# Kernel optimization log

Hardware: AMD Instinct MI355X
Metric: run time of the kernel (lower is better)

## Reference

```python
import jax, jax.numpy as jnp
import numpy as np

B, P, D_ENC, D_DEC, D_ATT, E, V, T = 64, 144, 1792, 512, 512, 300, 32000, 30
LN_EPS = 1e-5


def _ln(x, g, b):
    m = x.mean(-1, keepdims=True)
    v = jnp.var(x, axis=-1, keepdims=True)
    return (x - m) * jax.lax.rsqrt(v + LN_EPS) * g + b


def setup_inputs() -> dict:
    key = jax.random.key(0)
    ks = iter(jax.random.split(key, 40))
    r = lambda shape, s=0.02: (jax.random.normal(next(ks), shape, jnp.float32) * s)
    inp = {}
    inp['features'] = jax.random.normal(next(ks), (B, P, D_ENC), jnp.float32)
    inp['captions'] = jax.random.randint(next(ks), (B, T), 0, V, jnp.int32)
    inp['emb_table'] = r((V, E), 0.05)
    # attention params
    inp['ln_q_g'] = jnp.ones((D_DEC,), jnp.float32)
    inp['ln_q_b'] = jnp.zeros((D_DEC,), jnp.float32)
    inp['ln_kv_g'] = jnp.ones((D_ENC,), jnp.float32)
    inp['ln_kv_b'] = jnp.zeros((D_ENC,), jnp.float32)
    inp['Wq'] = r((D_DEC, D_ATT)); inp['bq'] = jnp.zeros((D_ATT,), jnp.float32)
    inp['Wk'] = r((D_ENC, D_ATT)); inp['bk'] = jnp.zeros((D_ATT,), jnp.float32)
    inp['Wbeta'] = r((D_DEC, 1)); inp['bbeta'] = jnp.zeros((1,), jnp.float32)
    # LSTM gate params, packed as [in_dim, 4*H] in gate order (i, f, o, g).
    # Context fed to the LSTM is the attention output of dim encoder_dim (V = normalized features).
    inp['Wh'] = r((D_DEC, 4 * D_DEC))
    inp['Wu'] = r((E, 4 * D_DEC))
    inp['Wa'] = r((D_ENC, 4 * D_DEC))
    inp['b_gates'] = jnp.zeros((4 * D_DEC,), jnp.float32)  # linear biases + extra b_* params combined
    # output head
    inp['W_Lh'] = r((D_DEC, E)); inp['b_Lh'] = jnp.zeros((E,), jnp.float32)
    inp['W_Lz'] = r((D_ENC, E)); inp['b_Lz'] = jnp.zeros((E,), jnp.float32)
    inp['W_Lo'] = r((E, V)); inp['b_Lo'] = jnp.zeros((V,), jnp.float32)
    # init state
    inp['W_ih'] = r((D_ENC, D_DEC)); inp['b_ih'] = jnp.zeros((D_DEC,), jnp.float32)
    inp['W_ic'] = r((D_ENC, D_DEC)); inp['b_ic'] = jnp.zeros((D_DEC,), jnp.float32)
    return inp


def reference(features, captions, emb_table, ln_q_g, ln_q_b, ln_kv_g, ln_kv_b,
              Wq, bq, Wk, bk, Wbeta, bbeta, Wh, Wu, Wa, b_gates,
              W_Lh, b_Lh, W_Lz, b_Lz, W_Lo, b_Lo, W_ih, b_ih, W_ic, b_ic):
    scale = jnp.sqrt(jnp.asarray(Wq.shape[1], jnp.float32))
    # features are constant across timesteps -> hoist ln_kv and K projection
    feats_n = _ln(features, ln_kv_g, ln_kv_b)          # [B,P,Denc]
    K = feats_n @ Wk + bk                               # [B,P,A]
    mean_a = features.mean(axis=1)                      # [B,Denc]
    h0 = mean_a @ W_ih + b_ih
    c0 = mean_a @ W_ic + b_ic
    embs = emb_table[captions]                          # [B,T,E] (dropout = identity in eval)
    xs = jnp.swapaxes(embs[:, :-1], 0, 1)               # [T-1,B,E], embedding at step t is word t-1

    def step(carry, emb_t):
        h, c = carry
        hq = _ln(h, ln_q_g, ln_q_b)                     # [B,H]
        Q = hq @ Wq + bq                                # [B,A]
        scores = jnp.einsum('ba,bpa->bp', Q, K) / scale
        alpha = jax.nn.softmax(scores, axis=-1)         # [B,P]
        context = jnp.einsum('bp,bpd->bd', alpha, feats_n)  # [B,Denc]
        beta = jax.nn.sigmoid(hq @ Wbeta + bbeta)       # [B,1]
        z = beta * context
        gates = h @ Wh + emb_t @ Wu + z @ Wa + b_gates  # [B,4H]
        i_t, f_t, o_t, g_t = jnp.split(gates, 4, axis=-1)
        c_new = jax.nn.sigmoid(f_t) * c + jax.nn.sigmoid(i_t) * jnp.tanh(g_t)
        h_new = jax.nn.sigmoid(o_t) * jnp.tanh(c_new)
        out_o = emb_t + (h_new @ W_Lh + b_Lh) + (z @ W_Lz + b_Lz)
        logits = out_o @ W_Lo + b_Lo                    # [B,V]
        return (h_new, c_new), (logits, alpha)

    _, (logits, alphas) = jax.lax.scan(step, (h0, c0), xs)
    # step t=0 stays zero, as in the original torch loop (range(1, seq_len))
    predictions = jnp.concatenate(
        [jnp.zeros((1,) + logits.shape[1:], logits.dtype), logits], axis=0).swapaxes(0, 1)
    alphas_out = jnp.concatenate(
        [jnp.zeros((1,) + alphas.shape[1:], alphas.dtype), alphas], axis=0).swapaxes(0, 1)
    return predictions, alphas_out
```

## Files before the change

kernel.cpp:

```cpp
#include <hip/hip_runtime.h>
#include <hip/hip_bf16.h>


#define NB 64
#define NP 144
#define DE 1792
#define DD 512
#define DA 512
#define EM 300
#define NV 32000
#define NTT 30
#define NS 29
#define G4 2048
#define KP 320
#define KG1 2304
#define LN_EPS 1e-5f
#define RSCALE 0.044194173824159216f
#define KSPL 12

typedef __attribute__((ext_vector_type(8))) short short8;
typedef __attribute__((ext_vector_type(4))) float f32x4;
typedef __attribute__((ext_vector_type(8))) unsigned short ushort8v;

__device__ __forceinline__ float bf2f(unsigned short u){
  union { unsigned int i; float f; } w; w.i = ((unsigned int)u) << 16; return w.f;
}
__device__ __forceinline__ unsigned short f2bf(float f){
  union { float f; unsigned int i; } u; u.f = f;
  unsigned int r = u.i + 0x7FFFu + ((u.i >> 16) & 1u);
  return (unsigned short)(r >> 16);
}
__device__ __forceinline__ float sigm(float x){ return 1.f/(1.f + __expf(-x)); }

__device__ __forceinline__ float wave_reduce_sum(float v){
  #pragma unroll
  for (int o = 32; o >= 1; o >>= 1) v += __shfl_xor(v, o);
  return v;
}
__device__ __forceinline__ float wave_reduce_max(float v){
  #pragma unroll
  for (int o = 32; o >= 1; o >>= 1) v = fmaxf(v, __shfl_xor(v, o));
  return v;
}
__device__ __forceinline__ float block_sum256(float v, float* sbuf){
  v = wave_reduce_sum(v);
  const int lane = threadIdx.x & 63, wid = threadIdx.x >> 6;
  if (lane == 0) sbuf[wid] = v;
  __syncthreads();
  const float r = sbuf[0] + sbuf[1] + sbuf[2] + sbuf[3];
  __syncthreads();
  return r;
}
__device__ __forceinline__ float block_sum512(float v, float* sbuf8){
  v = wave_reduce_sum(v);
  const int lane = threadIdx.x & 63, wid = threadIdx.x >> 6;
  if (lane == 0) sbuf8[wid] = v;
  __syncthreads();
  float r = 0.f;
  #pragma unroll
  for (int i = 0; i < 8; ++i) r += sbuf8[i];
  __syncthreads();
  return r;
}

__device__ __forceinline__ void stage_tile(const unsigned short* __restrict__ src,
    int row_stride, int k0, char* lds){
  const int tid = threadIdx.x;
  #pragma unroll
  for (int c = 0; c < 2; ++c){
    const int o = tid + c*256;
    const int m = o >> 3, ks8 = o & 7;
    const ushort8v v = *(const ushort8v*)&src[(size_t)m*row_stride + k0 + ks8*8];
    *(ushort8v*)&lds[m*128 + ((ks8 ^ (m&7))<<4)] = v;
  }
}
__device__ __forceinline__ void mma64(const char* Alds, const char* Blds,
    int w, int lane, f32x4 acc[4]){
  #pragma unroll
  for (int ks = 0; ks < 2; ++ks){
    const int slot = ks*4 + (lane>>4);
    const int n = w*16 + (lane&15);
    const short8 bfv = *(const short8*)&Blds[n*128 + ((slot ^ (n&7))<<4)];
    #pragma unroll
    for (int fm = 0; fm < 4; ++fm){
      const int m = fm*16 + (lane&15);
      const short8 afv = *(const short8*)&Alds[m*128 + ((slot ^ (m&7))<<4)];
      acc[fm] = __builtin_amdgcn_mfma_f32_16x16x32_bf16(afv, bfv, acc[fm], 0, 0, 0);
    }
  }
}

template <int NKT>
__device__ __forceinline__ void gemm_big(const unsigned short* __restrict__ A,
    const unsigned short* __restrict__ B, int sa, int sb,
    char* Alds, char* Blds, int mt, int nt, f32x4 acc[8][4]){
  const int tid = threadIdx.x, w = tid>>6, lane = tid&63;
  for (int kt = 0; kt < NKT; ++kt){
    const int k0 = kt*64;
    __syncthreads();
    #pragma unroll
    for (int c2 = 0; c2 < 4; ++c2){
      const int o16 = tid + c2*256;
      const int m = o16>>3, ks8 = o16&7;
      const ushort8v v = *(const ushort8v*)&A[(size_t)(mt*128+m)*sa + k0 + ks8*8];
      *(ushort8v*)&Alds[m*128 + ((ks8 ^ (m&7))<<4)] = v;
    }
    #pragma unroll
    for (int c2 = 0; c2 < 8; ++c2){
      const int o16 = tid + c2*256;
      const int n = o16>>3, ks8 = o16&7;
      const ushort8v v = *(const ushort8v*)&B[(size_t)(nt*256+n)*sb + k0 + ks8*8];
      *(ushort8v*)&Blds[n*128 + ((ks8 ^ (n&7))<<4)] = v;
    }
    __syncthreads();
    #pragma unroll
    for (int ks = 0; ks < 2; ++ks){
      const int slot = ks*4 + (lane>>4);
      short8 af[8];
      #pragma unroll
      for (int fm = 0; fm < 8; ++fm){
        const int m = fm*16 + (lane&15);
        af[fm] = *(const short8*)&Alds[m*128 + ((slot ^ (m&7))<<4)];
      }
      #pragma unroll
      for (int fn = 0; fn < 4; ++fn){
        const int n = w*64 + fn*16 + (lane&15);
        const short8 bfv = *(const short8*)&Blds[n*128 + ((slot ^ (n&7))<<4)];
        #pragma unroll
        for (int fm = 0; fm < 8; ++fm)
          acc[fm][fn] = __builtin_amdgcn_mfma_f32_16x16x32_bf16(af[fm], bfv, acc[fm][fn], 0, 0, 0);
      }
    }
  }
}

__global__ __launch_bounds__(256) void k_zero(float* __restrict__ pred,
                                              float* __restrict__ alph){
  const int idx = blockIdx.x * 256 + threadIdx.x;
  {
    const int b = idx / NV, v = idx - b * NV;
    pred[(size_t)b * NTT * NV + v] = 0.f;
  }
  if (idx < NB * NP){
    const int b = idx / NP, p = idx - b * NP;
    alph[(size_t)b * NTT * NP + p] = 0.f;
  }
}

__global__ __launch_bounds__(256) void k_ln_feats(const float* __restrict__ feats,
    const float* __restrict__ g, const float* __restrict__ bb,
    unsigned short* __restrict__ out){
  __shared__ float sbuf[4];
  const int row = blockIdx.x;
  const float* x = feats + (size_t)row * DE;
  float v[7]; float s = 0.f;
  #pragma unroll
  for (int i = 0; i < 7; ++i){ v[i] = x[i*256 + threadIdx.x]; s += v[i]; }
  const float mean = block_sum256(s, sbuf) * (1.f/DE);
  float q = 0.f;
  #pragma unroll
  for (int i = 0; i < 7; ++i){ const float d = v[i] - mean; q += d*d; }
  const float var = block_sum256(q, sbuf) * (1.f/DE);
  const float rinv = rsqrtf(var + LN_EPS);
  #pragma unroll
  for (int i = 0; i < 7; ++i){
    const int idx = i*256 + threadIdx.x;
    out[(size_t)row*DE + idx] = f2bf((v[i]-mean)*rinv*g[idx] + bb[idx]);
  }
}

__global__ __launch_bounds__(256) void k_mean(const float* __restrict__ feats,
                                              float* __restrict__ mean_a){
  const int idx = blockIdx.x * 256 + threadIdx.x;
  const int b = idx / DE, d = idx - b * DE;
  const float* p = feats + (size_t)b * NP * DE + d;
  float s = 0.f;
  for (int pp = 0; pp < NP; ++pp) s += p[(size_t)pp * DE];
  mean_a[idx] = s * (1.f/NP);
}

__global__ __launch_bounds__(256) void k_cvt_T(const float* __restrict__ src,
    unsigned short* __restrict__ dst, const int K, const int N, const int KPad){
  __shared__ float t[64][65];
  const int n0 = blockIdx.x*64, k0 = blockIdx.y*64;
  for (int i = threadIdx.x; i < 4096; i += 256){
    const int k = i>>6, n = i&63;
    t[k][n] = (k0 + k < K) ? src[(size_t)(k0+k)*N + n0+n] : 0.f;
  }
  __syncthreads();
  for (int i = threadIdx.x; i < 4096; i += 256){
    const int n = i>>6, k = i&63;
    dst[(size_t)(n0+n)*KPad + k0+k] = f2bf(t[k][n]);
  }
}

__global__ __launch_bounds__(256) void k_cvt_wlt(const float* __restrict__ W_Lh,
    const float* __restrict__ W_Lz, unsigned short* __restrict__ WLt){
  __shared__ float t[64][65];
  const int e0 = blockIdx.x*64, k0 = blockIdx.y*64;
  for (int i = threadIdx.x; i < 4096; i += 256){
    const int k = i>>6, e2 = i&63;
    const int kg = k0 + k, e = e0 + e2;
    float v = 0.f;
    if (e < EM) v = (kg < DD) ? W_Lh[(size_t)kg*EM + e] : W_Lz[(size_t)(kg-DD)*EM + e];
    t[k][e2] = v;
  }
  __syncthreads();
  for (int i = threadIdx.x; i < 4096; i += 256){
    const int e2 = i>>6, k = i&63;
    WLt[(size_t)(e0+e2)*KG1 + k0+k] = f2bf(t[k][e2]);
  }
}

__global__ __launch_bounds__(256) void k_wg(const float* __restrict__ Wq,
    const float* __restrict__ g, unsigned short* __restrict__ Wg){
  const int idx = blockIdx.x*256 + threadIdx.x;
  const int k = idx >> 9;
  Wg[idx] = f2bf(g[k]*Wq[idx]);
}

__global__ __launch_bounds__(512) void k_pre_vq(const float* __restrict__ Wq,
    const float* __restrict__ bk, float* __restrict__ vq){
  const int k = threadIdx.x;
  const float* row = Wq + (size_t)k*DA;
  float acc = 0.f;
  for (int a = 0; a < DA; ++a) acc = fmaf(row[a], bk[a], acc);
  vq[k] = acc;
}

__global__ __launch_bounds__(512) void k_uvoff(const float* __restrict__ Wq,
    const float* __restrict__ g, const float* __restrict__ bln,
    const float* __restrict__ bq, const float* __restrict__ Wbeta,
    const float* __restrict__ bbeta, const float* __restrict__ bk,
    float* __restrict__ u_, float* __restrict__ voff,
    float* __restrict__ gw, float* __restrict__ cscal){
  __shared__ float sbuf8[8];
  const int a = threadIdx.x;
  float uu = 0.f, vv = 0.f;
  for (int k = 0; k < DD; ++k){
    const float wv = Wq[(size_t)k*DA + a];
    uu = fmaf(g[k],   wv, uu);
    vv = fmaf(bln[k], wv, vv);
  }
  const float vo = vv + bq[a];
  u_[a]   = uu;
  voff[a] = vo;
  gw[a]   = g[a]*Wbeta[a];
  const float c1 = block_sum512(g[a]*Wbeta[a], sbuf8);
  const float c2 = block_sum512(bln[a]*Wbeta[a], sbuf8);
  const float c3 = block_sum512(uu*bk[a], sbuf8);
  const float c4 = block_sum512(vo*bk[a], sbuf8);
  if (a == 0){ cscal[0]=c1; cscal[1]=c2+bbeta[0]; cscal[2]=c3; cscal[3]=c4; }
}

__global__ __launch_bounds__(256) void k_KF(const unsigned short* __restrict__ fb,
    const unsigned short* __restrict__ WkT, unsigned short* __restrict__ KF){
  __shared__ char Alds[128*128];
  __shared__ char Blds[256*128];
  const int bid = blockIdx.x;
  const int wgid = (bid & 7)*18 + (bid >> 3);
  const int nt = wgid & 1, mt = wgid >> 1;
  const int tid = threadIdx.x, w = tid>>6, lane = tid&63;
  f32x4 acc[8][4];
  #pragma unroll
  for (int i = 0; i < 8; ++i)
    #pragma unroll
    for (int j = 0; j < 4; ++j) acc[i][j] = (f32x4)(0.f);
  gemm_big<28>(fb, WkT, DE, DE, Alds, Blds, mt, nt, acc);
  const int ncol0 = nt*256 + w*64 + (lane&15);
  #pragma unroll
  for (int fm = 0; fm < 8; ++fm)
    #pragma unroll
    for (int r = 0; r < 4; ++r){
      const int row = mt*128 + fm*16 + (lane>>4)*4 + r;
      #pragma unroll
      for (int fn = 0; fn < 4; ++fn)
        KF[(size_t)row*DD + ncol0 + fn*16] = f2bf(acc[fm][fn][r]);
    }
}

__global__ __launch_bounds__(256) void k_QG2(const unsigned short* __restrict__ KF,
    const unsigned short* __restrict__ Wg, const float* __restrict__ g_,
    const float* __restrict__ vq, unsigned short* __restrict__ G2){
  __shared__ char Alds[128*128];
  __shared__ char Blds[256*128];
  const int bid = blockIdx.x;
  const int wgid = (bid & 7)*18 + (bid >> 3);
  const int nt = wgid & 1, mt = wgid >> 1;
  const int tid = threadIdx.x, w = tid>>6, lane = tid&63;
  f32x4 acc[8][4];
  #pragma unroll
  for (int i = 0; i < 8; ++i)
    #pragma unroll
    for (int j = 0; j < 4; ++j) acc[i][j] = (f32x4)(0.f);
  gemm_big<8>(KF, Wg, DD, DD, Alds, Blds, mt, nt, acc);
  const int ncol0 = nt*256 + w*64 + (lane&15);
  float addv[4];
  #pragma unroll
  for (int fn = 0; fn < 4; ++fn){
    const int q = ncol0 + fn*16;
    addv[fn] = g_[q]*vq[q];
  }
  #pragma unroll
  for (int fm = 0; fm < 8; ++fm)
    #pragma unroll
    for (int r = 0; r < 4; ++r){
      const int row = mt*128 + fm*16 + (lane>>4)*4 + r;
      #pragma unroll
      for (int fn = 0; fn < 4; ++fn)
        G2[(size_t)row*DD + ncol0 + fn*16] = f2bf(acc[fm][fn][r] + addv[fn]);
    }
}

__global__ __launch_bounds__(512) void k_sc12(const unsigned short* __restrict__ KF,
    const float* __restrict__ u_, const float* __restrict__ voff,
    const float* __restrict__ cscal, float2* __restrict__ sc12){
  const int w = threadIdx.x>>6, lane = threadIdx.x&63;
  const int row = blockIdx.x*8 + w;
  const unsigned short* kf = KF + (size_t)row*DD + lane*8;
  float s1 = 0.f, s2 = 0.f;
  #pragma unroll
  for (int j = 0; j < 8; ++j){
    const float kv = bf2f(kf[j]);
    s1 = fmaf(u_[lane*8 + j],   kv, s1);
    s2 = fmaf(voff[lane*8 + j], kv, s2);
  }
  s1 = wave_reduce_sum(s1);
  s2 = wave_reduce_sum(s2);
  if (lane == 0){
    float2 o; o.x = s1 + cscal[2]; o.y = s2 + cscal[3];
    sc12[row] = o;
  }
}

__global__ __launch_bounds__(256) void k_init_g(const float* __restrict__ mean_a,
    const float* __restrict__ W, const float* __restrict__ bias,
    float* __restrict__ out, unsigned short* __restrict__ outbf){
  __shared__ float la[64*68];
  __shared__ float lb[64*68];
  const int j0 = blockIdx.x*64;
  const int tid = threadIdx.x, tr = tid&15, tn = tid>>4;
  float acc[16] = {0.f};
  for (int a0 = 0; a0 < DE; a0 += 64){
    __syncthreads();
    for (int i = tid; i < 4096; i += 256){
      const int b = i>>6, k = i&63;
      la[k*68 + b] = mean_a[(size_t)b*DE + a0+k];
    }
    for (int i = tid; i < 4096; i += 256){
      const int k = i>>6, j = i&63;
      lb[k*68 + j] = W[(size_t)(a0+k)*DD + j0+j];
    }
    __syncthreads();
    for (int k = 0; k < 64; ++k){
      float av[4], bv[4];
      #pragma unroll
      for (int ii = 0; ii < 4; ++ii) av[ii] = la[k*68 + tr*4+ii];
      #pragma unroll
      for (int jj = 0; jj < 4; ++jj) bv[jj] = lb[k*68 + tn*4+jj];
      #pragma unroll
      for (int ii = 0; ii < 4; ++ii)
        #pragma unroll
        for (int jj = 0; jj < 4; ++jj)
          acc[ii*4+jj] = fmaf(av[ii], bv[jj], acc[ii*4+jj]);
    }
  }
  #pragma unroll
  for (int ii = 0; ii < 4; ++ii)
    #pragma unroll
    for (int jj = 0; jj < 4; ++jj){
      const size_t idx = (size_t)(tr*4+ii)*DD + j0 + tn*4+jj;
      const float val = acc[ii*4+jj] + bias[j0 + tn*4+jj];
      out[idx] = val;
      if (outbf) outbf[idx] = f2bf(val);
    }
}

__global__ __launch_bounds__(256) void k_EU(const float* __restrict__ emb_table,
    const int* __restrict__ captions, const unsigned short* __restrict__ wut,
    float* __restrict__ eu){
  __shared__ char Alds[8192];
  __shared__ char Blds[8192];
  __shared__ int capL[64];
  const int jt = blockIdx.x, s = blockIdx.y;
  const int tid = threadIdx.x, w = tid>>6, lane = tid&63;
  if (tid < 64) capL[tid] = captions[tid*NTT + s];
  f32x4 acc[4];
  #pragma unroll
  for (int i = 0; i < 4; ++i) acc[i] = (f32x4)(0.f);
  for (int kt = 0; kt < 5; ++kt){
    __syncthreads();
    #pragma unroll
    for (int c = 0; c < 2; ++c){
      const int o = tid + c*256;
      const int m = o>>3, ks8 = o&7;
      const int e0 = kt*64 + ks8*8;
      const float* er = emb_table + (size_t)capL[m]*EM;
      ushort8v v;
      #pragma unroll
      for (int jj = 0; jj < 8; ++jj)
        v[jj] = (e0 + jj < EM) ? f2bf(er[e0 + jj]) : (unsigned short)0;
      *(ushort8v*)&Alds[m*128 + ((ks8 ^ (m&7))<<4)] = v;
    }
    stage_tile(wut + (size_t)jt*64*KP, KP, kt*64, Blds);
    __syncthreads();
    mma64(Alds, Blds, w, lane, acc);
  }
  const int j = jt*64 + w*16 + (lane&15);
  #pragma unroll
  for (int fm = 0; fm < 4; ++fm)
    #pragma unroll
    for (int r = 0; r < 4; ++r){
      const int b = fm*16 + (lane>>4)*4 + r;
      eu[((size_t)s*NB + b)*G4 + j] = acc[fm][r];
    }
}

__global__ __launch_bounds__(512) void k_A(
    const unsigned short* __restrict__ gp, const float* __restrict__ eu,
    const float* __restrict__ b_gates, const float* __restrict__ cin,
    float* __restrict__ cout, unsigned short* __restrict__ hst,
    const unsigned short* __restrict__ G2, const float2* __restrict__ sc12,
    const unsigned short* __restrict__ fb, const float* __restrict__ gw,
    const float* __restrict__ cscal, const int s, const int do_att,
    float* __restrict__ alph, unsigned short* __restrict__ zbf){
  __shared__ alignas(16) unsigned short hL[DD];
  __shared__ float sc[NP];
  __shared__ float al[NP];
  __shared__ float sredA[8*4];
  __shared__ float sbufM[8];
  __shared__ float sbufS[8];
  int sl, b;
  if (gridDim.x == 1){ sl = 0; b = blockIdx.y; }
  else {
    const int lin = blockIdx.x + 2*blockIdx.y;
    const int xcd = lin & 7, i = lin >> 3;
    b = xcd*8 + (i & 7);
    sl = i >> 3;
  }
  const int tid = threadIdx.x;
  const int w = tid>>6, lane = tid&63;
  float hn;
  if (s == 0){
    const unsigned short hb = hst[(size_t)b*DD + tid];
    hn = bf2f(hb);
    hL[tid] = hb;
  } else {
    const int m = s - 1;
    unsigned short gv[4*KSPL];
    #pragma unroll
    for (int ks = 0; ks < KSPL; ++ks){
      const unsigned short* gr = gp + ((size_t)ks*NB + b)*G4 + tid;
      gv[ks*4+0] = gr[0];
      gv[ks*4+1] = gr[DD];
      gv[ks*4+2] = gr[2*DD];
      gv[ks*4+3] = gr[3*DD];
    }
    const float* eur = eu + ((size_t)m*NB + b)*G4 + tid;
    float gs0 = b_gates[tid]        + eur[0];
    float gs1 = b_gates[DD + tid]   + eur[DD];
    float gs2 = b_gates[2*DD + tid] + eur[2*DD];
    float gs3 = b_gates[3*DD + tid] + eur[3*DD];
    #pragma unroll
    for (int ks = 0; ks < KSPL; ++ks){
      gs0 += bf2f(gv[ks*4+0]); gs1 += bf2f(gv[ks*4+1]);
      gs2 += bf2f(gv[ks*4+2]); gs3 += bf2f(gv[ks*4+3]);
    }
    const size_t idx = (size_t)b*DD + tid;
    const float cn = sigm(gs1)*cin[idx] + sigm(gs0)*tanhf(gs3);
    hn = sigm(gs2)*tanhf(cn);
    cout[idx] = cn;
    const unsigned short hb = f2bf(hn);
    hst[(size_t)s*NB*DD + idx] = hb;
    hL[tid] = hb;
  }
  if (!do_att) return;
  float p1 = hn, p2 = hn*hn, p3 = hn*gw[tid];
  #pragma unroll
  for (int o = 32; o >= 1; o >>= 1){
    p1 += __shfl_xor(p1, o);
    p2 += __shfl_xor(p2, o);
    p3 += __shfl_xor(p3, o);
  }
  if (lane == 0){ sredA[w*4] = p1; sredA[w*4+1] = p2; sredA[w*4+2] = p3; }
  __syncthreads();
  float S1 = 0.f, S2 = 0.f, S3 = 0.f;
  #pragma unroll
  for (int i = 0; i < 8; ++i){
    S1 += sredA[i*4]; S2 += sredA[i*4+1]; S3 += sredA[i*4+2];
  }
  const float mean = S1*(1.f/512.f);
  const float var  = S2*(1.f/512.f) - mean*mean;
  const float rinv = rsqrtf(var + LN_EPS);
  const float beta = sigm(rinv*(S3 - mean*cscal[0]) + cscal[1]);
  const short8 hv = *(const short8*)&hL[lane*8];
  #pragma unroll 1
  for (int i0 = 0; i0 < 18; i0 += 9){
    short8 U[9];
    float2 SV[9];
    #pragma unroll
    for (int j = 0; j < 9; ++j){
      const int p = w + 8*(i0+j);
      U[j] = *(const short8*)&G2[(size_t)(b*NP + p)*DD + lane*8];
      if (lane == 0) SV[j] = sc12[b*NP + p];
    }
    #pragma unroll
    for (int j = 0; j < 9; ++j){
      float a2 = 0.f;
      #pragma unroll
      for (int q = 0; q < 8; ++q)
        a2 = fmaf(bf2f((unsigned short)U[j][q]), bf2f((unsigned short)hv[q]), a2);
      a2 = wave_reduce_sum(a2);
      if (lane == 0)
        sc[w + 8*(i0+j)] = RSCALE*(rinv*a2 - rinv*mean*SV[j].x + SV[j].y);
    }
  }
  __syncthreads();
  const float v = (tid < NP) ? sc[tid] : -1e30f;
  const float mv = wave_reduce_max(v);
  if (lane == 0) sbufM[w] = mv;
  __syncthreads();
  float mm = sbufM[0];
  #pragma unroll
  for (int i = 1; i < 8; ++i) mm = fmaxf(mm, sbufM[i]);
  const float e = (tid < NP) ? __expf(v - mm) : 0.f;
  const float sv = wave_reduce_sum(e);
  if (lane == 0) sbufS[w] = sv;
  __syncthreads();
  float ssum = 0.f;
  #pragma unroll
  for (int i = 0; i < 8; ++i) ssum += sbufS[i];
  if (tid < NP){
    const float a3 = e / ssum;
    al[tid] = a3;
    if (sl == 0) alph[((size_t)b*NTT + s + 1)*NP + tid] = a3;
  }
  __syncthreads();
  if (tid < 448){
    const int d0 = sl*896 + tid*2;
    const unsigned short* fB = fb + (size_t)b*NP*DE + d0;
    float a0 = 0.f, a1 = 0.f;
    #pragma unroll 1
    for (int p0 = 0; p0 < NP; p0 += 36){
      ushort2 fv[36];
      #pragma unroll
      for (int j = 0; j < 36; ++j) fv[j] = *(const ushort2*)&fB[(size_t)(p0+j)*DE];
      #pragma unroll
      for (int j = 0; j < 36; ++j){
        const float ap = al[p0+j];
        a0 = fmaf(ap, bf2f(fv[j].x), a0);
        a1 = fmaf(ap, bf2f(fv[j].y), a1);
      }
    }
    ushort2 zo;
    zo.x = f2bf(a0*beta);
    zo.y = f2bf(a1*beta);
    *(ushort2*)&zbf[((size_t)s*NB + b)*DE + d0] = zo;
  }
}

__global__ __launch_bounds__(256) void k_B(
    const unsigned short* __restrict__ hst, const unsigned short* __restrict__ zbf,
    const unsigned short* __restrict__ whT, const unsigned short* __restrict__ wat,
    const int s, unsigned short* __restrict__ gp){
  __shared__ char Alds[8192];
  __shared__ char Blds[8192];
  const int jt = blockIdx.x, ks = blockIdx.y;
  const int tid = threadIdx.x, w = tid>>6, lane = tid&63;
  const unsigned short* hrow = hst + (size_t)s*NB*DD;
  const unsigned short* zrow = zbf + (size_t)s*NB*DE;
  f32x4 acc[4];
  #pragma unroll
  for (int i = 0; i < 4; ++i) acc[i] = (f32x4)(0.f);
  for (int kt = 0; kt < 3; ++kt){
    const int k0 = ks*192 + kt*64;
    __syncthreads();
    if (k0 < DD) stage_tile(hrow, DD, k0, Alds);
    else         stage_tile(zrow, DE, k0 - DD, Alds);
    #pragma unroll
    for (int c2 = 0; c2 < 2; ++c2){
      const int o = tid + c2*256;
      const int m = o>>3, ks8 = o&7;
      const int col = (m>>4)*DD + jt*16 + (m&15);
      const unsigned short* src = (k0 < DD)
          ? whT + (size_t)col*DD + k0
          : wat + (size_t)col*DE + (k0 - DD);
      const ushort8v v = *(const ushort8v*)&src[ks8*8];
      *(ushort8v*)&Blds[m*128 + ((ks8 ^ (m&7))<<4)] = v;
    }
    __syncthreads();
    mma64(Alds, Blds, w, lane, acc);
  }
  const int jcol = jt*16 + (lane&15);
  unsigned short* gps = gp + (size_t)ks*NB*G4;
  #pragma unroll
  for (int fm = 0; fm < 4; ++fm)
    #pragma unroll
    for (int r = 0; r < 4; ++r){
      const int b = fm*16 + (lane>>4)*4 + r;
      gps[(size_t)b*G4 + w*DD + jcol] = f2bf(acc[fm][r]);
    }
}

__global__ __launch_bounds__(256) void k_G1m(const unsigned short* __restrict__ hstbf,
    const unsigned short* __restrict__ zbf, const unsigned short* __restrict__ WLt,
    float* __restrict__ g1p){
  __shared__ char Alds[8192];
  __shared__ char Blds[8192];
  const int e0 = blockIdx.x*64, s = blockIdx.y, ks6 = blockIdx.z;
  const int tid = threadIdx.x, w = tid>>6, lane = tid&63;
  const unsigned short* hrow = hstbf + (size_t)(s+1)*NB*DD;
  const unsigned short* zrow = zbf + (size_t)s*NB*DE;
  f32x4 acc[4];
  #pragma unroll
  for (int i = 0; i < 4; ++i) acc[i] = (f32x4)(0.f);
  for (int kt = 0; kt < 6; ++kt){
    const int k0 = ks6*384 + kt*64;
    __syncthreads();
    if (k0 < DD) stage_tile(hrow, DD, k0, Alds);
    else         stage_tile(zrow, DE, k0 - DD, Alds);
    stage_tile(WLt + (size_t)e0*KG1, KG1, k0, Blds);
    __syncthreads();
    mma64(Alds, Blds, w, lane, acc);
  }
  const int e = e0 + w*16 + (lane&15);
  float* dst = g1p + (size_t)ks6*NS*NB*KP;
  #pragma unroll
  for (int fm = 0; fm < 4; ++fm)
    #pragma unroll
    for (int r = 0; r < 4; ++r){
      const int b = fm*16 + (lane>>4)*4 + r;
      dst[((size_t)s*NB + b)*KP + e] = acc[fm][r];
    }
}

__global__ __launch_bounds__(256) void k_G1red(const float* __restrict__ g1p,
    const float* __restrict__ b_Lh, const float* __restrict__ b_Lz,
    const float* __restrict__ emb_table, const int* __restrict__ captions,
    unsigned short* __restrict__ outo){
  const int idx = blockIdx.x*256 + threadIdx.x;
  const int row = idx / KP, e = idx - row*KP;
  const int s = row >> 6, b = row & 63;
  float v = 0.f;
  #pragma unroll
  for (int ks6 = 0; ks6 < 6; ++ks6) v += g1p[(size_t)ks6*NS*NB*KP + idx];
  if (e < EM){
    const int cap = captions[b*NTT + s];
    v += b_Lh[e] + b_Lz[e] + emb_table[(size_t)cap*EM + e];
  } else v = 0.f;
  outo[idx] = f2bf(v);
}

__global__ __launch_bounds__(256) void k_G2(const unsigned short* __restrict__ Abf,
    const unsigned short* __restrict__ Bt, const float* __restrict__ b_Lo,
    float* __restrict__ pred){
  __shared__ char Alds[128*128];
  __shared__ char Blds[256*128];
  const int bid = blockIdx.x;
  const int xcd = bid & 7, idx8 = bid >> 3;
  const int wgid = (xcd < 3 ? xcd*235 : 705 + (xcd-3)*234) + idx8;
  const int nt = wgid / 15, mt = wgid - nt*15;
  const int tid = threadIdx.x, w = tid>>6, lane = tid&63;
  f32x4 acc[8][4];
  #pragma unroll
  for (int i = 0; i < 8; ++i)
    #pragma unroll
    for (int j = 0; j < 4; ++j)
      acc[i][j] = (f32x4)(0.f);
  gemm_big<5>(Abf, Bt, KP, KP, Alds, Blds, mt, nt, acc);
  const int ncol0 = nt*256 + w*64 + (lane&15);
  #pragma unroll
  for (int fm = 0; fm < 8; ++fm){
    #pragma unroll
    for (int r = 0; r < 4; ++r){
      const int row = mt*128 + fm*16 + (lane>>4)*4 + r;
      if (row < NS*NB){
        const int s = row >> 6, b = row & 63;
        float* prow = &pred[((size_t)b*NTT + s + 1)*NV + ncol0];
        #pragma unroll
        for (int fn = 0; fn < 4; ++fn)
          __builtin_nontemporal_store(acc[fm][fn][r] + b_Lo[ncol0 + fn*16],
                                      &prow[fn*16]);
      }
    }
  }
}

extern "C" void kernel_launch(void* const* d_in, const int* in_sizes, int n_in,
                              void* d_out, int out_size, void* d_ws, size_t ws_size,
                              hipStream_t stream){
  const float* features  = (const float*)d_in[0];
  const int*   captions  = (const int*)  d_in[1];
  const float* emb_table = (const float*)d_in[2];
  const float* ln_q_g = (const float*)d_in[3];
  const float* ln_q_b = (const float*)d_in[4];
  const float* ln_kv_g= (const float*)d_in[5];
  const float* ln_kv_b= (const float*)d_in[6];
  const float* Wq     = (const float*)d_in[7];
  const float* bq     = (const float*)d_in[8];
  const float* Wk     = (const float*)d_in[9];
  const float* bk     = (const float*)d_in[10];
  const float* Wbeta  = (const float*)d_in[11];
  const float* bbeta  = (const float*)d_in[12];
  const float* Wh     = (const float*)d_in[13];
  const float* Wu     = (const float*)d_in[14];
  const float* Wa     = (const float*)d_in[15];
  const float* b_gates= (const float*)d_in[16];
  const float* W_Lh   = (const float*)d_in[17];
  const float* b_Lh   = (const float*)d_in[18];
  const float* W_Lz   = (const float*)d_in[19];
  const float* b_Lz   = (const float*)d_in[20];
  const float* W_Lo   = (const float*)d_in[21];
  const float* b_Lo   = (const float*)d_in[22];
  const float* W_ih   = (const float*)d_in[23];
  const float* b_ih   = (const float*)d_in[24];
  const float* W_ic   = (const float*)d_in[25];
  const float* b_ic   = (const float*)d_in[26];

  float* pred = (float*)d_out;
  float* alph = pred + (size_t)NB * NTT * NV;

  char* w = (char*)d_ws;
  auto alloc = [&](size_t bytes) -> void* {
    void* p = (void*)w; w += (bytes + 255) & ~(size_t)255; return p;
  };
  unsigned short* feats_bf = (unsigned short*)alloc((size_t)NB*NP*DE * 2);
  unsigned short* wlo_t    = (unsigned short*)alloc((size_t)NV*KP * 2);
  unsigned short* whT      = (unsigned short*)alloc((size_t)G4*DD * 2);
  unsigned short* wut      = (unsigned short*)alloc((size_t)G4*KP * 2);
  unsigned short* wat      = (unsigned short*)alloc((size_t)G4*DE * 2);
  unsigned short* WkT      = (unsigned short*)alloc((size_t)DD*DE * 2);
  unsigned short* WLt      = (unsigned short*)alloc((size_t)KP*KG1 * 2);
  unsigned short* Wg       = (unsigned short*)alloc((size_t)DD*DD * 2);
  unsigned short* KFbf     = (unsigned short*)alloc((size_t)NB*NP*DD * 2);
  unsigned short* G2bf     = (unsigned short*)alloc((size_t)NB*NP*DD * 2);
  float2* sc12  = (float2*)alloc((size_t)NB*NP * 8);
  float* vq     = (float*)alloc((size_t)DD * 4);
  float* u_     = (float*)alloc((size_t)DD * 4);
  float* voff   = (float*)alloc((size_t)DD * 4);
  float* gw     = (float*)alloc((size_t)DD * 4);
  float* cscal  = (float*)alloc(16);
  float* mean_a = (float*)alloc((size_t)NB*DE * 4);
  float* hbuf   = (float*)alloc((size_t)NB*DD * 4);
  float* cb0    = (float*)alloc((size_t)NB*DD * 4);
  float* cb1    = (float*)alloc((size_t)NB*DD * 4);
  unsigned short* hstbf = (unsigned short*)alloc((size_t)(NS+1)*NB*DD * 2);
  unsigned short* zbf   = (unsigned short*)alloc((size_t)NS*NB*DE * 2);
  unsigned short* outo  = (unsigned short*)alloc((size_t)1920*KP * 2);
  unsigned short* gp    = (unsigned short*)alloc((size_t)KSPL*NB*G4 * 2);
  float* eu_all = (float*)alloc((size_t)NS*NB*G4 * 4);
  float* g1p    = (float*)alloc((size_t)6*NS*NB*KP * 4);
  float* cb[2] = { cb0, cb1 };

  k_zero<<<dim3((NB*NV)/256), dim3(256), 0, stream>>>(pred, alph);
  k_ln_feats<<<dim3(NB*NP), dim3(256), 0, stream>>>(features, ln_kv_g, ln_kv_b, feats_bf);
  k_mean<<<dim3((NB*DE)/256), dim3(256), 0, stream>>>(features, mean_a);
  k_cvt_T<<<dim3(NV/64, KP/64), dim3(256), 0, stream>>>(W_Lo, wlo_t, EM, NV, KP);
  k_cvt_T<<<dim3(G4/64, DD/64), dim3(256), 0, stream>>>(Wh, whT, DD, G4, DD);
  k_cvt_T<<<dim3(G4/64, KP/64), dim3(256), 0, stream>>>(Wu, wut, EM, G4, KP);
  k_cvt_T<<<dim3(G4/64, DE/64), dim3(256), 0, stream>>>(Wa, wat, DE, G4, DE);
  k_cvt_T<<<dim3(DD/64, DE/64), dim3(256), 0, stream>>>(Wk, WkT, DE, DD, DE);
  k_cvt_wlt<<<dim3(KP/64, KG1/64), dim3(256), 0, stream>>>(W_Lh, W_Lz, WLt);
  k_wg<<<dim3((DD*DD)/256), dim3(256), 0, stream>>>(Wq, ln_q_g, Wg);
  k_pre_vq<<<dim3(1), dim3(512), 0, stream>>>(Wq, bk, vq);
  k_uvoff<<<dim3(1), dim3(512), 0, stream>>>(Wq, ln_q_g, ln_q_b, bq, Wbeta, bbeta,
      bk, u_, voff, gw, cscal);
  k_KF<<<dim3(144), dim3(256), 0, stream>>>(feats_bf, WkT, KFbf);
  k_QG2<<<dim3(144), dim3(256), 0, stream>>>(KFbf, Wg, ln_q_g, vq, G2bf);
  k_sc12<<<dim3(NB*NP/8), dim3(512), 0, stream>>>(KFbf, u_, voff, cscal, sc12);
  k_init_g<<<dim3(DD/64), dim3(256), 0, stream>>>(mean_a, W_ih, b_ih, hbuf, hstbf);
  k_init_g<<<dim3(DD/64), dim3(256), 0, stream>>>(mean_a, W_ic, b_ic, cb0, nullptr);
  k_EU<<<dim3(G4/64, NS), dim3(256), 0, stream>>>(emb_table, captions, wut, eu_all);

  for (int s = 0; s < NS; ++s){
    k_A<<<dim3(2, NB), dim3(512), 0, stream>>>(gp, eu_all, b_gates,
        cb[(s & 1) ^ 1], cb[s & 1], hstbf, G2bf, sc12, feats_bf,
        gw, cscal, s, 1, alph, zbf);
    k_B<<<dim3(32, KSPL), dim3(256), 0, stream>>>(hstbf, zbf, whT, wat, s, gp);
  }
  k_A<<<dim3(1, NB), dim3(512), 0, stream>>>(gp, eu_all, b_gates,
      cb[(NS & 1) ^ 1], cb[NS & 1], hstbf, G2bf, sc12, feats_bf,
      gw, cscal, NS, 0, alph, zbf);

  k_G1m<<<dim3(5, NS, 6), dim3(256), 0, stream>>>(hstbf, zbf, WLt, g1p);
  k_G1red<<<dim3((NS*NB*KP)/256), dim3(256), 0, stream>>>(g1p, b_Lh, b_Lz,
      emb_table, captions, outo);
  k_G2<<<dim3(1875), dim3(256), 0, stream>>>(outo, wlo_t, b_Lo, pred);
}
```

Baseline: 1.284 ms.

## Merge setup conversion kernels and retile output-head GEMM into 128x256 blocks

Six weight transpose/convert launches are merged into one kernel that dispatches on block index. The vq and u/voff prep kernels and the two init-state GEMMs are also merged, cutting the setup launch count. The k_G1m projection GEMM changes from 64x64 tiles per timestep to 128x256 tiles over the flattened (step,batch) rows, with swizzled LDS and more MFMAs per tile to improve reuse. The trade-off is a larger accumulator register footprint and some padded work at the row and column edges.

```diff
diff --git a/kernel.cpp b/kernel.cpp
--- a/kernel.cpp
+++ b/kernel.cpp
@@ -179,10 +179,40 @@
   mean_a[idx] = s * (1.f/NP);
 }
 
-__global__ __launch_bounds__(256) void k_cvt_T(const float* __restrict__ src,
-    unsigned short* __restrict__ dst, const int K, const int N, const int KPad){
+__global__ __launch_bounds__(256) void k_cvt_all(
+    const float* __restrict__ W_Lo, const float* __restrict__ Wh,
+    const float* __restrict__ Wu,  const float* __restrict__ Wa,
+    const float* __restrict__ Wk,  const float* __restrict__ W_Lh,
+    const float* __restrict__ W_Lz,
+    unsigned short* __restrict__ wlo_t, unsigned short* __restrict__ whT,
+    unsigned short* __restrict__ wut,   unsigned short* __restrict__ wat,
+    unsigned short* __restrict__ WkT,   unsigned short* __restrict__ WLt){
   __shared__ float t[64][65];
-  const int n0 = blockIdx.x*64, k0 = blockIdx.y*64;
+  int lb = blockIdx.x;
+  if (lb >= 4036){
+    lb -= 4036;
+    const int e0 = (lb % 5)*64, k0 = (lb / 5)*64;
+    for (int i = threadIdx.x; i < 4096; i += 256){
+      const int k = i>>6, e2 = i&63;
+      const int kg = k0 + k, e = e0 + e2;
+      float v = 0.f;
+      if (e < EM) v = (kg < DD) ? W_Lh[(size_t)kg*EM + e] : W_Lz[(size_t)(kg-DD)*EM + e];
+      t[k][e2] = v;
+    }
+    __syncthreads();
+    for (int i = threadIdx.x; i < 4096; i += 256){
+      const int e2 = i>>6, k = i&63;
+      WLt[(size_t)(e0+e2)*KG1 + k0+k] = f2bf(t[k][e2]);
+    }
+    return;
+  }
+  const float* src; unsigned short* dst; int K, N, KPad, nx;
+  if      (lb < 2500){             src=W_Lo; dst=wlo_t; K=EM; N=NV; KPad=KP; nx=500; }
+  else if (lb < 2756){ lb -= 2500; src=Wh;   dst=whT;   K=DD; N=G4; KPad=DD; nx=32; }
+  else if (lb < 2916){ lb -= 2756; src=Wu;   dst=wut;   K=EM; N=G4; KPad=KP; nx=32; }
+  else if (lb < 3812){ lb -= 2916; src=Wa;   dst=wat;   K=DE; N=G4; KPad=DE; nx=32; }
+  else               { lb -= 3812; src=Wk;   dst=WkT;   K=DE; N=DD; KPad=DE; nx=8;  }
+  const int n0 = (lb % nx)*64, k0 = (lb / nx)*64;
   for (int i = threadIdx.x; i < 4096; i += 256){
     const int k = i>>6, n = i&63;
     t[k][n] = (k0 + k < K) ? src[(size_t)(k0+k)*N + n0+n] : 0.f;
@@ -191,24 +221,6 @@
   for (int i = threadIdx.x; i < 4096; i += 256){
     const int n = i>>6, k = i&63;
     dst[(size_t)(n0+n)*KPad + k0+k] = f2bf(t[k][n]);
-  }
-}
-
-__global__ __launch_bounds__(256) void k_cvt_wlt(const float* __restrict__ W_Lh,
-    const float* __restrict__ W_Lz, unsigned short* __restrict__ WLt){
-  __shared__ float t[64][65];
-  const int e0 = blockIdx.x*64, k0 = blockIdx.y*64;
-  for (int i = threadIdx.x; i < 4096; i += 256){
-    const int k = i>>6, e2 = i&63;
-    const int kg = k0 + k, e = e0 + e2;
-    float v = 0.f;
-    if (e < EM) v = (kg < DD) ? W_Lh[(size_t)kg*EM + e] : W_Lz[(size_t)(kg-DD)*EM + e];
-    t[k][e2] = v;
-  }
-  __syncthreads();
-  for (int i = threadIdx.x; i < 4096; i += 256){
-    const int e2 = i>>6, k = i&63;
-    WLt[(size_t)(e0+e2)*KG1 + k0+k] = f2bf(t[k][e2]);
   }
 }
 
@@ -219,23 +231,21 @@
   Wg[idx] = f2bf(g[k]*Wq[idx]);
 }
 
-__global__ __launch_bounds__(512) void k_pre_vq(const float* __restrict__ Wq,
-    const float* __restrict__ bk, float* __restrict__ vq){
-  const int k = threadIdx.x;
-  const float* row = Wq + (size_t)k*DA;
-  float acc = 0.f;
-  for (int a = 0; a < DA; ++a) acc = fmaf(row[a], bk[a], acc);
-  vq[k] = acc;
-}
-
-__global__ __launch_bounds__(512) void k_uvoff(const float* __restrict__ Wq,
-    const float* __restrict__ g, const float* __restrict__ bln,
-    const float* __restrict__ bq, const float* __restrict__ Wbeta,
-    const float* __restrict__ bbeta, const float* __restrict__ bk,
-    float* __restrict__ u_, float* __restrict__ voff,
-    float* __restrict__ gw, float* __restrict__ cscal){
+__global__ __launch_bounds__(512) void k_prep(const float* __restrict__ Wq,
+    const float* __restrict__ bk, const float* __restrict__ g,
+    const float* __restrict__ bln, const float* __restrict__ bq,
+    const float* __restrict__ Wbeta, const float* __restrict__ bbeta,
+    float* __restrict__ vq, float* __restrict__ u_,
+    float* __restrict__ voff, float* __restrict__ gw,
+    float* __restrict__ cscal){
   __shared__ float sbuf8[8];
   const int a = threadIdx.x;
+  {
+    const float* row = Wq + (size_t)a*DA;
+    float acc = 0.f;
+    for (int j = 0; j < DA; ++j) acc = fmaf(row[j], bk[j], acc);
+    vq[a] = acc;
+  }
   float uu = 0.f, vv = 0.f;
   for (int k = 0; k < DD; ++k){
     const float wv = Wq[(size_t)k*DA + a];
@@ -334,10 +344,17 @@
 }
 
 __global__ __launch_bounds__(256) void k_init_g(const float* __restrict__ mean_a,
-    const float* __restrict__ W, const float* __restrict__ bias,
-    float* __restrict__ out, unsigned short* __restrict__ outbf){
+    const float* __restrict__ W_ih, const float* __restrict__ b_ih,
+    const float* __restrict__ W_ic, const float* __restrict__ b_ic,
+    float* __restrict__ hbuf, unsigned short* __restrict__ hstbf,
+    float* __restrict__ cb0){
   __shared__ float la[64*68];
   __shared__ float lb[64*68];
+  const int which = blockIdx.y;
+  const float* W    = which ? W_ic : W_ih;
+  const float* bias = which ? b_ic : b_ih;
+  float* out = which ? cb0 : hbuf;
+  unsigned short* outbf = which ? nullptr : hstbf;
   const int j0 = blockIdx.x*64;
   const int tid = threadIdx.x, tr = tid&15, tn = tid>>4;
   float acc[16] = {0.f};
@@ -605,33 +622,81 @@
 __global__ __launch_bounds__(256) void k_G1m(const unsigned short* __restrict__ hstbf,
     const unsigned short* __restrict__ zbf, const unsigned short* __restrict__ WLt,
     float* __restrict__ g1p){
-  __shared__ char Alds[8192];
-  __shared__ char Blds[8192];
-  const int e0 = blockIdx.x*64, s = blockIdx.y, ks6 = blockIdx.z;
+  __shared__ char Alds[128*128];
+  __shared__ char Blds[256*128];
+  const int mt = blockIdx.x, nt = blockIdx.y, ks6 = blockIdx.z;
   const int tid = threadIdx.x, w = tid>>6, lane = tid&63;
-  const unsigned short* hrow = hstbf + (size_t)(s+1)*NB*DD;
-  const unsigned short* zrow = zbf + (size_t)s*NB*DE;
-  f32x4 acc[4];
-  #pragma unroll
-  for (int i = 0; i < 4; ++i) acc[i] = (f32x4)(0.f);
+  f32x4 acc[8][4];
+  #pragma unroll
+  for (int i = 0; i < 8; ++i)
+    #pragma unroll
+    for (int j = 0; j < 4; ++j) acc[i][j] = (f32x4)(0.f);
   for (int kt = 0; kt < 6; ++kt){
     const int k0 = ks6*384 + kt*64;
     __syncthreads();
-    if (k0 < DD) stage_tile(hrow, DD, k0, Alds);
-    else         stage_tile(zrow, DE, k0 - DD, Alds);
-    stage_tile(WLt + (size_t)e0*KG1, KG1, k0, Blds);
-    __syncthreads();
-    mma64(Alds, Blds, w, lane, acc);
-  }
-  const int e = e0 + w*16 + (lane&15);
+    #pragma unroll
+    for (int c2 = 0; c2 < 4; ++c2){
+      const int o16 = tid + c2*256;
+      const int m = o16>>3, ks8 = o16&7;
+      const int r = mt*128 + m;
+      ushort8v v;
+      if (r < NS*NB){
+        const int sS = r >> 6, bb = r & 63;
+        const unsigned short* srcp = (k0 < DD)
+            ? hstbf + ((size_t)(sS+1)*NB + bb)*DD + k0
+            : zbf + ((size_t)sS*NB + bb)*DE + (k0 - DD);
+        v = *(const ushort8v*)&srcp[ks8*8];
+      } else {
+        #pragma unroll
+        for (int j = 0; j < 8; ++j) v[j] = 0;
+      }
+      *(ushort8v*)&Alds[m*128 + ((ks8 ^ (m&7))<<4)] = v;
+    }
+    #pragma unroll
+    for (int c2 = 0; c2 < 8; ++c2){
+      const int o16 = tid + c2*256;
+      const int n = o16>>3, ks8 = o16&7;
+      int nr = nt*256 + n;
+      if (nr >= KP) nr = KP - 1;
+      const ushort8v v = *(const ushort8v*)&WLt[(size_t)nr*KG1 + k0 + ks8*8];
+      *(ushort8v*)&Blds[n*128 + ((ks8 ^ (n&7))<<4)] = v;
+    }
+    __syncthreads();
+    #pragma unroll
+    for (int ks = 0; ks < 2; ++ks){
+      const int slot = ks*4 + (lane>>4);
+      short8 af[8];
+      #pragma unroll
+      for (int fm = 0; fm < 8; ++fm){
+        const int m = fm*16 + (lane&15);
+        af[fm] = *(const short8*)&Alds[m*128 + ((slot ^ (m&7))<<4)];
+      }
+      #pragma unroll
+      for (int fn = 0; fn < 4; ++fn){
+        const int n = w*64 + fn*16 + (lane&15);
+        const short8 bfv = *(const short8*)&Blds[n*128 + ((slot ^ (n&7))<<4)];
+        #pragma unroll
+        for (int fm = 0; fm < 8; ++fm)
+          acc[fm][fn] = __builtin_amdgcn_mfma_f32_16x16x32_bf16(af[fm], bfv, acc[fm][fn], 0, 0, 0);
+      }
+    }
+  }
+  const int ncol0 = nt*256 + w*64 + (lane&15);
   float* dst = g1p + (size_t)ks6*NS*NB*KP;
   #pragma unroll
-  for (int fm = 0; fm < 4; ++fm)
+  for (int fm = 0; fm < 8; ++fm){
     #pragma unroll
     for (int r = 0; r < 4; ++r){
-      const int b = fm*16 + (lane>>4)*4 + r;
-      dst[((size_t)s*NB + b)*KP + e] = acc[fm][r];
-    }
+      const int row = mt*128 + fm*16 + (lane>>4)*4 + r;
+      if (row < NS*NB){
+        #pragma unroll
+        for (int fn = 0; fn < 4; ++fn){
+          const int e = ncol0 + fn*16;
+          if (e < KP) dst[(size_t)row*KP + e] = acc[fm][fn][r];
+        }
+      }
+    }
+  }
 }
 
 __global__ __launch_bounds__(256) void k_G1red(const float* __restrict__ g1p,
@@ -755,21 +820,16 @@
   k_zero<<<dim3((NB*NV)/256), dim3(256), 0, stream>>>(pred, alph);
   k_ln_feats<<<dim3(NB*NP), dim3(256), 0, stream>>>(features, ln_kv_g, ln_kv_b, feats_bf);
   k_mean<<<dim3((NB*DE)/256), dim3(256), 0, stream>>>(features, mean_a);
-  k_cvt_T<<<dim3(NV/64, KP/64), dim3(256), 0, stream>>>(W_Lo, wlo_t, EM, NV, KP);
-  k_cvt_T<<<dim3(G4/64, DD/64), dim3(256), 0, stream>>>(Wh, whT, DD, G4, DD);
-  k_cvt_T<<<dim3(G4/64, KP/64), dim3(256), 0, stream>>>(Wu, wut, EM, G4, KP);
-  k_cvt_T<<<dim3(G4/64, DE/64), dim3(256), 0, stream>>>(Wa, wat, DE, G4, DE);
-  k_cvt_T<<<dim3(DD/64, DE/64), dim3(256), 0, stream>>>(Wk, WkT, DE, DD, DE);
-  k_cvt_wlt<<<dim3(KP/64, KG1/64), dim3(256), 0, stream>>>(W_Lh, W_Lz, WLt);
+  k_cvt_all<<<dim3(4216), dim3(256), 0, stream>>>(W_Lo, Wh, Wu, Wa, Wk, W_Lh, W_Lz,
+      wlo_t, whT, wut, wat, WkT, WLt);
   k_wg<<<dim3((DD*DD)/256), dim3(256), 0, stream>>>(Wq, ln_q_g, Wg);
-  k_pre_vq<<<dim3(1), dim3(512), 0, stream>>>(Wq, bk, vq);
-  k_uvoff<<<dim3(1), dim3(512), 0, stream>>>(Wq, ln_q_g, ln_q_b, bq, Wbeta, bbeta,
-      bk, u_, voff, gw, cscal);
+  k_prep<<<dim3(1), dim3(512), 0, stream>>>(Wq, bk, ln_q_g, ln_q_b, bq, Wbeta,
+      bbeta, vq, u_, voff, gw, cscal);
   k_KF<<<dim3(144), dim3(256), 0, stream>>>(feats_bf, WkT, KFbf);
   k_QG2<<<dim3(144), dim3(256), 0, stream>>>(KFbf, Wg, ln_q_g, vq, G2bf);
   k_sc12<<<dim3(NB*NP/8), dim3(512), 0, stream>>>(KFbf, u_, voff, cscal, sc12);
-  k_init_g<<<dim3(DD/64), dim3(256), 0, stream>>>(mean_a, W_ih, b_ih, hbuf, hstbf);
-  k_init_g<<<dim3(DD/64), dim3(256), 0, stream>>>(mean_a, W_ic, b_ic, cb0, nullptr);
+  k_init_g<<<dim3(DD/64, 2), dim3(256), 0, stream>>>(mean_a, W_ih, b_ih, W_ic, b_ic,
+      hbuf, hstbf, cb0);
   k_EU<<<dim3(G4/64, NS), dim3(256), 0, stream>>>(emb_table, captions, wut, eu_all);
 
   for (int s = 0; s < NS; ++s){
@@ -782,7 +842,7 @@
       cb[(NS & 1) ^ 1], cb[NS & 1], hstbf, G2bf, sc12, feats_bf,
       gw, cscal, NS, 0, alph, zbf);
 
-  k_G1m<<<dim3(5, NS, 6), dim3(256), 0, stream>>>(hstbf, zbf, WLt, g1p);
+  k_G1m<<<dim3(15, 2, 6), dim3(256), 0, stream>>>(hstbf, zbf, WLt, g1p);
   k_G1red<<<dim3((NS*NB*KP)/256), dim3(256), 0, stream>>>(g1p, b_Lh, b_Lz,
       emb_table, captions, outo);
   k_G2<<<dim3(1875), dim3(256), 0, stream>>>(outo, wlo_t, b_Lo, pred);
```

Result: faster. 1.143 ms (-11.0%).
